# Optimization experiments

Hardware: AMD Instinct MI355X
Metric: run time of the kernel (lower is better)

## Reference

```python
import jax, jax.numpy as jnp
import numpy as np

B, IN_DIM, HID, ATT = 16384, 128, 512, 256
TOTAL = IN_DIM + HID + ATT


def setup_inputs() -> dict:
    key = jax.random.key(0)
    ks = jax.random.split(key, 10)
    u = lambda k, shape, lo, hi: jax.random.uniform(k, shape, jnp.float32, lo, hi)
    return {
        "t": jnp.float32(0.0),
        "h_ltc": jax.random.normal(ks[0], (B, HID), jnp.float32),
        "x_t": jax.random.normal(ks[1], (B, IN_DIM), jnp.float32),
        "context": jax.random.normal(ks[2], (B, ATT), jnp.float32),
        "W_gd": u(ks[3], (2 * HID, TOTAL), -0.1, 0.1),
        "b_gd": u(ks[4], (2 * HID,), -0.1, 0.1),
        "W_tau": u(ks[5], (HID, HID), -0.1, 0.1),
        "b_tau": u(ks[6], (HID,), -0.1, 0.1),
        "gleak": u(ks[7], (HID,), 0.001, 1.0),
        "cm": u(ks[8], (HID,), 0.4, 0.6),
    }


def reference(t, h_ltc, x_t, context, W_gd, b_gd, W_tau, b_tau, gleak, cm):
    # combined: [B, IN+HID+ATT]
    combined = jnp.concatenate([x_t, h_ltc, context], axis=1)
    g_d = combined @ W_gd.T + b_gd            # [B, 2*HID]
    gate, dynamics = jnp.split(g_d, 2, axis=1)
    tau = jax.nn.softplus(h_ltc @ W_tau.T + b_tau)  # [B, HID]
    numerator = jax.nn.sigmoid(gate) * jnp.tanh(dynamics) - h_ltc
    denominator = tau + jax.nn.softplus(cm) + jax.nn.softplus(gleak)
    return numerator / (denominator + 1e-6)
```

## Files before the change

### kernel.cpp

```cpp
#include <hip/hip_runtime.h>
#include <hip/hip_bf16.h>
#include <math.h>

#define BROWS 16384
#define IN_DIM 128
#define HID 512
#define ATT 256
#define KTOT 896
#define KC_TOT 112

typedef __bf16 bf16x8 __attribute__((ext_vector_type(8)));
typedef float f32x4 __attribute__((ext_vector_type(4)));

__global__ void pack_A(const float* __restrict__ x, const float* __restrict__ h,
                       const float* __restrict__ ctx, __hip_bfloat16* __restrict__ A_stage) {
    const int mt = blockIdx.x;
    const int kb = blockIdx.y;
    const float* src; int rs, c0;
    if (kb == 0)      { src = x;   rs = IN_DIM; c0 = 0; }
    else if (kb < 5)  { src = h;   rs = HID;    c0 = (kb - 1) * 128; }
    else              { src = ctx; rs = ATT;    c0 = (kb - 5) * 128; }

    __shared__ __attribute__((aligned(16))) __hip_bfloat16 tile[128][136];

    const int tid = threadIdx.x;
    #pragma unroll
    for (int it = 0; it < 16; ++it) {
        int lin = it * 256 + tid;
        int mi = lin >> 5;
        int c4 = lin & 31;
        float4 v = *(const float4*)(src + (size_t)(mt * 128 + mi) * rs + c0 + c4 * 4);
        union { __hip_bfloat16 hh[4]; ushort4 u; } p;
        p.hh[0] = __float2bfloat16(v.x);
        p.hh[1] = __float2bfloat16(v.y);
        p.hh[2] = __float2bfloat16(v.z);
        p.hh[3] = __float2bfloat16(v.w);
        *(ushort4*)&tile[mi][c4 * 4] = p.u;
    }
    __syncthreads();
    #pragma unroll
    for (int it = 0; it < 8; ++it) {
        int lin = it * 256 + tid;
        int kcl = lin >> 7;
        int mi  = lin & 127;
        uint4 vv = *(const uint4*)&tile[mi][kcl * 8];
        *(uint4*)(A_stage + ((size_t)(mt * KC_TOT + kb * 16 + kcl) * 128 + mi) * 8) = vv;
    }
}

__device__ __forceinline__ float softplus_f(float x) {
    return fmaxf(x, 0.0f) + log1pf(__expf(-fabsf(x)));
}

__global__ void pack_B(const float* __restrict__ W_gd, const float* __restrict__ W_tau,
                       const float* __restrict__ gleak, const float* __restrict__ cm,
                       __hip_bfloat16* __restrict__ B_stage, float* __restrict__ dconst) {
    const int cid = blockIdx.x * 256 + threadIdx.x;
    if (cid < HID) {
        dconst[cid] = softplus_f(cm[cid]) + softplus_f(gleak[cid]) + 1e-6f;
    }
    const int nl = cid % 192;
    const int kc = (cid / 192) % KC_TOT;
    const int jt = cid / (192 * KC_TOT);
    const int jg = nl / 48, type = (nl % 48) / 16, j16 = nl % 16;
    const int j = jt * 64 + jg * 16 + j16;
    const int k0 = kc * 8;

    float v[8];
    if (type == 0) {
        const float* s = W_gd + (size_t)j * KTOT + k0;
        #pragma unroll
        for (int i = 0; i < 8; ++i) v[i] = s[i];
    } else if (type == 1) {
        const float* s = W_gd + (size_t)(HID + j) * KTOT + k0;
        #pragma unroll
        for (int i = 0; i < 8; ++i) v[i] = s[i];
    } else {
        if (k0 >= IN_DIM && k0 < IN_DIM + HID) {
            const float* s = W_tau + (size_t)j * HID + (k0 - IN_DIM);
            #pragma unroll
            for (int i = 0; i < 8; ++i) v[i] = s[i];
        } else {
            #pragma unroll
            for (int i = 0; i < 8; ++i) v[i] = 0.0f;
        }
    }
    union { __hip_bfloat16 hh[8]; uint4 u; } p;
    #pragma unroll
    for (int i = 0; i < 8; ++i) p.hh[i] = __float2bfloat16(v[i]);
    *(uint4*)(B_stage + (size_t)cid * 8) = p.u;
}

__global__ __launch_bounds__(256, 2) void ltc_gemm(
    const __hip_bfloat16* __restrict__ A_stage, const __hip_bfloat16* __restrict__ B_stage,
    const float* __restrict__ h_ltc, const float* __restrict__ b_gd,
    const float* __restrict__ b_tau, const float* __restrict__ dconst,
    float* __restrict__ out) {

    __shared__ __attribute__((aligned(16))) char smem[16384 + 24576];
    char* As = smem;
    char* Bs = smem + 16384;

    const int bx = blockIdx.x;
    const int mt = bx & 127;
    const int jt = bx >> 7;
    const int tid = threadIdx.x;
    const int wave = tid >> 6, lane = tid & 63;
    const int wm = wave >> 1;
    const int wj = wave & 1;
    const int q = lane >> 4, t = lane & 15;

    f32x4 accg[2][4], accd[2][4], acct[2][4];
    #pragma unroll
    for (int g = 0; g < 2; ++g)
        #pragma unroll
        for (int i = 0; i < 4; ++i) {
            accg[g][i] = (f32x4)0.0f; accd[g][i] = (f32x4)0.0f; acct[g][i] = (f32x4)0.0f;
        }

    const __hip_bfloat16* aSrc[4]; char* aDst[4];
    #pragma unroll
    for (int r = 0; r < 4; ++r) {
        int c = wave + 4 * r;
        int kcl = c >> 1, half = c & 1;
        aSrc[r] = A_stage + ((size_t)(mt * KC_TOT + kcl) * 128 + half * 64 + lane) * 8;
        aDst[r] = As + c * 1024;
    }
    const __hip_bfloat16* bSrc[6]; char* bDst[6];
    #pragma unroll
    for (int r = 0; r < 6; ++r) {
        int c = wave + 4 * r;
        bSrc[r] = B_stage + (size_t)jt * (KC_TOT * 1536) + c * 512 + lane * 8;
        bDst[r] = Bs + c * 1024;
    }

    for (int ks = 0; ks < 14; ++ks) {
        #pragma unroll
        for (int r = 0; r < 4; ++r)
            __builtin_amdgcn_global_load_lds(
                (const __attribute__((address_space(1))) void*)aSrc[r],
                (__attribute__((address_space(3))) void*)aDst[r], 16, 0, 0);
        #pragma unroll
        for (int r = 0; r < 6; ++r)
            __builtin_amdgcn_global_load_lds(
                (const __attribute__((address_space(1))) void*)bSrc[r],
                (__attribute__((address_space(3))) void*)bDst[r], 16, 0, 0);
        __syncthreads();

        const bool tau_on = (ks >= 2 && ks < 10);
        #pragma unroll
        for (int ko2 = 0; ko2 < 2; ++ko2) {
            const int kcl = ko2 * 4 + q;
            const char* ab = As + (((kcl * 128) + wm * 64 + t) << 4);
            bf16x8 a0 = *(const bf16x8*)(ab);
            bf16x8 a1 = *(const bf16x8*)(ab + 256);
            bf16x8 a2 = *(const bf16x8*)(ab + 512);
            bf16x8 a3 = *(const bf16x8*)(ab + 768);
            #pragma unroll
            for (int g = 0; g < 2; ++g) {
                const char* bb = Bs + (((kcl * 192) + wj * 96 + g * 48 + t) << 4);
                bf16x8 bg = *(const bf16x8*)(bb);
                bf16x8 bd = *(const bf16x8*)(bb + 256);
                accg[g][0] = __builtin_amdgcn_mfma_f32_16x16x32_bf16(a0, bg, accg[g][0], 0, 0, 0);
                accg[g][1] = __builtin_amdgcn_mfma_f32_16x16x32_bf16(a1, bg, accg[g][1], 0, 0, 0);
                accg[g][2] = __builtin_amdgcn_mfma_f32_16x16x32_bf16(a2, bg, accg[g][2], 0, 0, 0);
                accg[g][3] = __builtin_amdgcn_mfma_f32_16x16x32_bf16(a3, bg, accg[g][3], 0, 0, 0);
                accd[g][0] = __builtin_amdgcn_mfma_f32_16x16x32_bf16(a0, bd, accd[g][0], 0, 0, 0);
                accd[g][1] = __builtin_amdgcn_mfma_f32_16x16x32_bf16(a1, bd, accd[g][1], 0, 0, 0);
                accd[g][2] = __builtin_amdgcn_mfma_f32_16x16x32_bf16(a2, bd, accd[g][2], 0, 0, 0);
                accd[g][3] = __builtin_amdgcn_mfma_f32_16x16x32_bf16(a3, bd, accd[g][3], 0, 0, 0);
                if (tau_on) {
                    bf16x8 bt = *(const bf16x8*)(bb + 512);
                    acct[g][0] = __builtin_amdgcn_mfma_f32_16x16x32_bf16(a0, bt, acct[g][0], 0, 0, 0);
                    acct[g][1] = __builtin_amdgcn_mfma_f32_16x16x32_bf16(a1, bt, acct[g][1], 0, 0, 0);
                    acct[g][2] = __builtin_amdgcn_mfma_f32_16x16x32_bf16(a2, bt, acct[g][2], 0, 0, 0);
                    acct[g][3] = __builtin_amdgcn_mfma_f32_16x16x32_bf16(a3, bt, acct[g][3], 0, 0, 0);
                }
            }
        }
        #pragma unroll
        for (int r = 0; r < 4; ++r) aSrc[r] += 8192;
        #pragma unroll
        for (int r = 0; r < 6; ++r) bSrc[r] += 12288;
        __syncthreads();
    }

    const int row0 = mt * 128 + wm * 64 + q * 4;
    #pragma unroll
    for (int g = 0; g < 2; ++g) {
        const int j = jt * 64 + (wj * 2 + g) * 16 + t;
        const float bgj = b_gd[j];
        const float bdj = b_gd[HID + j];
        const float btj = b_tau[j];
        const float dcj = dconst[j];
        #pragma unroll
        for (int i = 0; i < 4; ++i) {
            #pragma unroll
            for (int r = 0; r < 4; ++r) {
                const int row = row0 + i * 16 + r;
                const float gv = accg[g][i][r] + bgj;
                const float dv = accd[g][i][r] + bdj;
                const float tp = acct[g][i][r] + btj;
                const float h  = h_ltc[(size_t)row * HID + j];
                const float sig = __builtin_amdgcn_rcpf(1.0f + __expf(-gv));
                const float th  = 1.0f - 2.0f * __builtin_amdgcn_rcpf(__expf(2.0f * dv) + 1.0f);
                const float tau = fmaxf(tp, 0.0f) + __logf(1.0f + __expf(-fabsf(tp)));
                out[(size_t)row * HID + j] = (sig * th - h) * __builtin_amdgcn_rcpf(tau + dcj);
            }
        }
    }
}

extern "C" void kernel_launch(void* const* d_in, const int* in_sizes, int n_in,
                              void* d_out, int out_size, void* d_ws, size_t ws_size,
                              hipStream_t stream) {
    const float* h_ltc = (const float*)d_in[1];
    const float* x_t   = (const float*)d_in[2];
    const float* ctx   = (const float*)d_in[3];
    const float* W_gd  = (const float*)d_in[4];
    const float* b_gd  = (const float*)d_in[5];
    const float* W_tau = (const float*)d_in[6];
    const float* b_tau = (const float*)d_in[7];
    const float* gleak = (const float*)d_in[8];
    const float* cm    = (const float*)d_in[9];

    char* ws = (char*)d_ws;
    __hip_bfloat16* A_stage = (__hip_bfloat16*)ws;
    __hip_bfloat16* B_stage = (__hip_bfloat16*)(ws + 29360128);
    float* dconst = (float*)(ws + 29360128 + 2752512);

    pack_B<<<672, 256, 0, stream>>>(W_gd, W_tau, gleak, cm, B_stage, dconst);
    pack_A<<<dim3(128, 7), 256, 0, stream>>>(x_t, h_ltc, ctx, A_stage);
    ltc_gemm<<<1024, 256, 0, stream>>>(A_stage, B_stage, h_ltc, b_gd, b_tau, dconst,
                                       (float*)d_out);
}
```

Measured before the change: 170.7 us.

## Fuse activation bf16 packing into GEMM with register prefetch and XOR-swizzled LDS

Removes the separate pack_A kernel and its bf16 staging buffer. The GEMM now reads fp32 x/h/context directly, converts to bf16 in registers, and writes to LDS using an XOR swizzle to avoid bank conflicts. The next K-slab is prefetched into registers while the current one is computed. Launch bounds move to 3 blocks per SM. This saves one kernel launch and a full write plus read of the staged A matrix. In exchange, each of the 8 column-tile blocks re-reads the fp32 A data, so global read traffic roughly doubles and register pressure goes up.

```diff
diff --git a/kernel.cpp b/kernel.cpp
--- a/kernel.cpp
+++ b/kernel.cpp
@@ -12,42 +12,6 @@
 typedef __bf16 bf16x8 __attribute__((ext_vector_type(8)));
 typedef float f32x4 __attribute__((ext_vector_type(4)));
 
-__global__ void pack_A(const float* __restrict__ x, const float* __restrict__ h,
-                       const float* __restrict__ ctx, __hip_bfloat16* __restrict__ A_stage) {
-    const int mt = blockIdx.x;
-    const int kb = blockIdx.y;
-    const float* src; int rs, c0;
-    if (kb == 0)      { src = x;   rs = IN_DIM; c0 = 0; }
-    else if (kb < 5)  { src = h;   rs = HID;    c0 = (kb - 1) * 128; }
-    else              { src = ctx; rs = ATT;    c0 = (kb - 5) * 128; }
-
-    __shared__ __attribute__((aligned(16))) __hip_bfloat16 tile[128][136];
-
-    const int tid = threadIdx.x;
-    #pragma unroll
-    for (int it = 0; it < 16; ++it) {
-        int lin = it * 256 + tid;
-        int mi = lin >> 5;
-        int c4 = lin & 31;
-        float4 v = *(const float4*)(src + (size_t)(mt * 128 + mi) * rs + c0 + c4 * 4);
-        union { __hip_bfloat16 hh[4]; ushort4 u; } p;
-        p.hh[0] = __float2bfloat16(v.x);
-        p.hh[1] = __float2bfloat16(v.y);
-        p.hh[2] = __float2bfloat16(v.z);
-        p.hh[3] = __float2bfloat16(v.w);
-        *(ushort4*)&tile[mi][c4 * 4] = p.u;
-    }
-    __syncthreads();
-    #pragma unroll
-    for (int it = 0; it < 8; ++it) {
-        int lin = it * 256 + tid;
-        int kcl = lin >> 7;
-        int mi  = lin & 127;
-        uint4 vv = *(const uint4*)&tile[mi][kcl * 8];
-        *(uint4*)(A_stage + ((size_t)(mt * KC_TOT + kb * 16 + kcl) * 128 + mi) * 8) = vv;
-    }
-}
-
 __device__ __forceinline__ float softplus_f(float x) {
     return fmaxf(x, 0.0f) + log1pf(__expf(-fabsf(x)));
 }
@@ -91,11 +55,19 @@
     *(uint4*)(B_stage + (size_t)cid * 8) = p.u;
 }
 
-__global__ __launch_bounds__(256, 2) void ltc_gemm(
-    const __hip_bfloat16* __restrict__ A_stage, const __hip_bfloat16* __restrict__ B_stage,
-    const float* __restrict__ h_ltc, const float* __restrict__ b_gd,
-    const float* __restrict__ b_tau, const float* __restrict__ dconst,
-    float* __restrict__ out) {
+__device__ __forceinline__ void slab_src(int ks, const float* x, const float* h,
+                                         const float* c, const float*& src,
+                                         int& rs, int& c0) {
+    if (ks < 2)       { src = x; rs = IN_DIM; c0 = ks * 64; }
+    else if (ks < 10) { src = h; rs = HID;    c0 = (ks - 2) * 64; }
+    else              { src = c; rs = ATT;    c0 = (ks - 10) * 64; }
+}
+
+__global__ __launch_bounds__(256, 3) void ltc_gemm(
+    const float* __restrict__ x, const float* __restrict__ h_ltc,
+    const float* __restrict__ ctx, const __hip_bfloat16* __restrict__ B_stage,
+    const float* __restrict__ b_gd, const float* __restrict__ b_tau,
+    const float* __restrict__ dconst, float* __restrict__ out) {
 
     __shared__ __attribute__((aligned(16))) char smem[16384 + 24576];
     char* As = smem;
@@ -110,6 +82,9 @@
     const int wj = wave & 1;
     const int q = lane >> 4, t = lane & 15;
 
+    const int kc8 = tid & 7;
+    const int mi0 = tid >> 3;
+
     f32x4 accg[2][4], accd[2][4], acct[2][4];
     #pragma unroll
     for (int g = 0; g < 2; ++g)
@@ -118,14 +93,6 @@
             accg[g][i] = (f32x4)0.0f; accd[g][i] = (f32x4)0.0f; acct[g][i] = (f32x4)0.0f;
         }
 
-    const __hip_bfloat16* aSrc[4]; char* aDst[4];
-    #pragma unroll
-    for (int r = 0; r < 4; ++r) {
-        int c = wave + 4 * r;
-        int kcl = c >> 1, half = c & 1;
-        aSrc[r] = A_stage + ((size_t)(mt * KC_TOT + kcl) * 128 + half * 64 + lane) * 8;
-        aDst[r] = As + c * 1024;
-    }
     const __hip_bfloat16* bSrc[6]; char* bDst[6];
     #pragma unroll
     for (int r = 0; r < 6; ++r) {
@@ -134,12 +101,33 @@
         bDst[r] = Bs + c * 1024;
     }
 
+    float4 pf[4][2];
+    {
+        const float* src; int rs, c0;
+        slab_src(0, x, h_ltc, ctx, src, rs, c0);
+        #pragma unroll
+        for (int r = 0; r < 4; ++r) {
+            const float* p = src + (size_t)(mt * 128 + mi0 + 32 * r) * rs + c0 + kc8 * 8;
+            pf[r][0] = *(const float4*)p;
+            pf[r][1] = *(const float4*)(p + 4);
+        }
+    }
+
     for (int ks = 0; ks < 14; ++ks) {
         #pragma unroll
-        for (int r = 0; r < 4; ++r)
-            __builtin_amdgcn_global_load_lds(
-                (const __attribute__((address_space(1))) void*)aSrc[r],
-                (__attribute__((address_space(3))) void*)aDst[r], 16, 0, 0);
+        for (int r = 0; r < 4; ++r) {
+            union { __hip_bfloat16 hh[8]; uint4 u; } pk;
+            pk.hh[0] = __float2bfloat16(pf[r][0].x);
+            pk.hh[1] = __float2bfloat16(pf[r][0].y);
+            pk.hh[2] = __float2bfloat16(pf[r][0].z);
+            pk.hh[3] = __float2bfloat16(pf[r][0].w);
+            pk.hh[4] = __float2bfloat16(pf[r][1].x);
+            pk.hh[5] = __float2bfloat16(pf[r][1].y);
+            pk.hh[6] = __float2bfloat16(pf[r][1].z);
+            pk.hh[7] = __float2bfloat16(pf[r][1].w);
+            const int mi = mi0 + 32 * r;
+            *(uint4*)(As + ((kc8 * 128 + (mi ^ kc8)) << 4)) = pk.u;
+        }
         #pragma unroll
         for (int r = 0; r < 6; ++r)
             __builtin_amdgcn_global_load_lds(
@@ -147,11 +135,22 @@
                 (__attribute__((address_space(3))) void*)bDst[r], 16, 0, 0);
         __syncthreads();
 
+        if (ks < 13) {
+            const float* src; int rs, c0;
+            slab_src(ks + 1, x, h_ltc, ctx, src, rs, c0);
+            #pragma unroll
+            for (int r = 0; r < 4; ++r) {
+                const float* p = src + (size_t)(mt * 128 + mi0 + 32 * r) * rs + c0 + kc8 * 8;
+                pf[r][0] = *(const float4*)p;
+                pf[r][1] = *(const float4*)(p + 4);
+            }
+        }
+
         const bool tau_on = (ks >= 2 && ks < 10);
         #pragma unroll
         for (int ko2 = 0; ko2 < 2; ++ko2) {
             const int kcl = ko2 * 4 + q;
-            const char* ab = As + (((kcl * 128) + wm * 64 + t) << 4);
+            const char* ab = As + ((kcl * 128 + ((wm * 64 + t) ^ kcl)) << 4);
             bf16x8 a0 = *(const bf16x8*)(ab);
             bf16x8 a1 = *(const bf16x8*)(ab + 256);
             bf16x8 a2 = *(const bf16x8*)(ab + 512);
@@ -179,8 +178,6 @@
             }
         }
         #pragma unroll
-        for (int r = 0; r < 4; ++r) aSrc[r] += 8192;
-        #pragma unroll
         for (int r = 0; r < 6; ++r) bSrc[r] += 12288;
         __syncthreads();
     }
@@ -201,11 +198,11 @@
                 const float gv = accg[g][i][r] + bgj;
                 const float dv = accd[g][i][r] + bdj;
                 const float tp = acct[g][i][r] + btj;
-                const float h  = h_ltc[(size_t)row * HID + j];
+                const float hv = h_ltc[(size_t)row * HID + j];
                 const float sig = __builtin_amdgcn_rcpf(1.0f + __expf(-gv));
                 const float th  = 1.0f - 2.0f * __builtin_amdgcn_rcpf(__expf(2.0f * dv) + 1.0f);
                 const float tau = fmaxf(tp, 0.0f) + __logf(1.0f + __expf(-fabsf(tp)));
-                out[(size_t)row * HID + j] = (sig * th - h) * __builtin_amdgcn_rcpf(tau + dcj);
+                out[(size_t)row * HID + j] = (sig * th - hv) * __builtin_amdgcn_rcpf(tau + dcj);
             }
         }
     }
@@ -225,12 +222,10 @@
     const float* cm    = (const float*)d_in[9];
 
     char* ws = (char*)d_ws;
-    __hip_bfloat16* A_stage = (__hip_bfloat16*)ws;
-    __hip_bfloat16* B_stage = (__hip_bfloat16*)(ws + 29360128);
-    float* dconst = (float*)(ws + 29360128 + 2752512);
+    __hip_bfloat16* B_stage = (__hip_bfloat16*)ws;
+    float* dconst = (float*)(ws + 2752512);
 
     pack_B<<<672, 256, 0, stream>>>(W_gd, W_tau, gleak, cm, B_stage, dconst);
-    pack_A<<<dim3(128, 7), 256, 0, stream>>>(x_t, h_ltc, ctx, A_stage);
-    ltc_gemm<<<1024, 256, 0, stream>>>(A_stage, B_stage, h_ltc, b_gd, b_tau, dconst,
+    ltc_gemm<<<1024, 256, 0, stream>>>(x_t, h_ltc, ctx, B_stage, b_gd, b_tau, dconst,
                                        (float*)d_out);
 }
```

Result: slower. 237.4 us (+39.1%).
